# Kernel optimization log

Hardware: AMD Instinct MI355X
Metric: run time of the kernel (lower is better)

Reference implementation:

```python
import jax, jax.numpy as jnp
import numpy as np

DIM = 1024
INTER = 1408
N_EXPERTS = 16
TOPK = 2
N_SHARED = 2
SHARED_INTER = N_SHARED * INTER
ROUTE_SCALE = 1.0


def setup_inputs() -> dict:
    key = jax.random.key(0)
    ks = jax.random.split(key, 16)
    s = 0.02
    return {
        "x": jax.random.normal(ks[0], (2, 2048, DIM), dtype=jnp.float32),
        "gate_w": jax.random.normal(ks[1], (DIM, N_EXPERTS), dtype=jnp.float32) * s,
        "gate_b": jnp.zeros((N_EXPERTS,), dtype=jnp.float32),
        "w1": jax.random.normal(ks[2], (N_EXPERTS, DIM, INTER), dtype=jnp.float32) * s,
        "b1": jnp.zeros((N_EXPERTS, INTER), dtype=jnp.float32),
        "w3": jax.random.normal(ks[3], (N_EXPERTS, DIM, INTER), dtype=jnp.float32) * s,
        "b3": jnp.zeros((N_EXPERTS, INTER), dtype=jnp.float32),
        "w2": jax.random.normal(ks[4], (N_EXPERTS, INTER, DIM), dtype=jnp.float32) * s,
        "b2": jnp.zeros((N_EXPERTS, DIM), dtype=jnp.float32),
        "sw1": jax.random.normal(ks[5], (DIM, SHARED_INTER), dtype=jnp.float32) * s,
        "sb1": jax.random.normal(ks[6], (SHARED_INTER,), dtype=jnp.float32) * s,
        "sw3": jax.random.normal(ks[7], (DIM, SHARED_INTER), dtype=jnp.float32) * s,
        "sb3": jax.random.normal(ks[8], (SHARED_INTER,), dtype=jnp.float32) * s,
        "sw2": jax.random.normal(ks[9], (SHARED_INTER, DIM), dtype=jnp.float32) * s,
        "sb2": jax.random.normal(ks[10], (DIM,), dtype=jnp.float32) * s,
    }


def reference(x, gate_w, gate_b, w1, b1, w3, b3, w2, b2, sw1, sb1, sw3, sb3, sw2, sb2):
    shape = x.shape
    xf = x.reshape(-1, DIM)  # [T, D]

    # Gate: softmax scores in fp32, top-k routing
    logits = xf @ gate_w + gate_b  # [T, E]
    scores = jax.nn.softmax(logits.astype(jnp.float32), axis=-1)
    top_vals, top_idx = jax.lax.top_k(scores, TOPK)  # [T, K]
    weights = (top_vals * ROUTE_SCALE).astype(x.dtype)

    # Combine weights per expert: [T, E]; zero for unselected experts
    cw = (jax.nn.one_hot(top_idx, N_EXPERTS, dtype=x.dtype) * weights[..., None]).sum(axis=1)

    # Routed experts (dense-per-expert SwiGLU, masked by combine weights)
    h = jnp.einsum('td,edh->teh', xf, w1) + b1  # [T, E, I]
    g = jnp.einsum('td,edh->teh', xf, w3) + b3
    a = jax.nn.silu(h) * g
    y = jnp.einsum('teh,ehd,te->td', a, w2, cw) + cw @ b2  # [T, D]

    # Shared expert SwiGLU
    z = (jax.nn.silu(xf @ sw1 + sb1) * (xf @ sw3 + sb3)) @ sw2 + sb2

    return (y + z).reshape(shape)
```

## Files before the change

### kernel.cpp

```cpp
#include <hip/hip_runtime.h>
#include <cstdint>
#include <cstddef>

#define T_TOKENS 4096
#define DIM      1024
#define INTER    1408
#define NEXP     16
#define SINTER   2816

typedef uint32_t u32;
typedef uint16_t u16;

using s8v = __attribute__((ext_vector_type(8))) short;
using f4v = __attribute__((ext_vector_type(4))) float;

__device__ __forceinline__ u16 f2bf(float f) {
  u32 u = __float_as_uint(f);
  return (u16)((u + 0x7fffu + ((u >> 16) & 1u)) >> 16);
}
__device__ __forceinline__ u32 pack2(float a, float b) {
  return (u32)f2bf(a) | ((u32)f2bf(b) << 16);
}

__device__ __forceinline__ void load_lds16(const u16* g, u16* l) {
  __builtin_amdgcn_global_load_lds((const __attribute__((address_space(1))) void*)g,
                                   (__attribute__((address_space(3))) void*)l,
                                   16, 0, 0);
}

__global__ __launch_bounds__(256)
void cvt_x(const float* __restrict__ in, u16* __restrict__ out) {
  const int i = (blockIdx.x * 256 + threadIdx.x) * 8;
  float4 a = *(const float4*)(in + i);
  float4 b = *(const float4*)(in + i + 4);
  uint4 o;
  o.x = pack2(a.x, a.y); o.y = pack2(a.z, a.w);
  o.z = pack2(b.x, b.y); o.w = pack2(b.z, b.w);
  *(uint4*)(out + i) = o;
}

__global__ __launch_bounds__(256)
void transpose_cvt(const float* __restrict__ in, u16* __restrict__ out,
                   int K, int N) {
  const size_t eoff = (size_t)blockIdx.z * K * N;
  const int n0 = blockIdx.x * 64, k0 = blockIdx.y * 64;
  __shared__ u16 t[64][72];

  const int tid = threadIdx.x;
  {
    const int r = tid >> 4, c4 = (tid & 15) * 4;
    const float* src = in + eoff + (size_t)k0 * N + n0;
#pragma unroll
    for (int i = 0; i < 4; i++) {
      int row = r + i * 16;
      float4 v = *(const float4*)(src + (size_t)row * N + c4);
      t[c4 + 0][row] = f2bf(v.x);
      t[c4 + 1][row] = f2bf(v.y);
      t[c4 + 2][row] = f2bf(v.z);
      t[c4 + 3][row] = f2bf(v.w);
    }
  }
  __syncthreads();
  {
    const int r = tid >> 3, cc = (tid & 7) * 8;
    u16* dst = out + eoff + (size_t)n0 * K + k0;
#pragma unroll
    for (int i = 0; i < 2; i++) {
      int row = r + i * 32;
      uint4 v = *(const uint4*)&t[row][cc];
      *(uint4*)(dst + (size_t)row * K + cc) = v;
    }
  }
}

__global__ __launch_bounds__(256)
void gate_logits(const float* __restrict__ x, const float* __restrict__ gw,
                 const float* __restrict__ gb,
                 int* __restrict__ g_e, float* __restrict__ g_w)
{
  const int tok  = blockIdx.x * 4 + (threadIdx.x >> 6);
  const int lane = threadIdx.x & 63;
  const int e = lane & 15, s = lane >> 4;
  const float* xr = x + (size_t)tok * DIM;

  float acc = 0.f;
#pragma unroll 8
  for (int i = 0; i < DIM / 4; i++) {
    const int k = i * 4 + s;
    acc = fmaf(xr[k], gw[i * 64 + lane], acc);
  }
  acc += __shfl_xor(acc, 16, 64);
  acc += __shfl_xor(acc, 32, 64);
  const float logit = acc + gb[e];

  float mx = logit;
#pragma unroll
  for (int o = 1; o < 16; o <<= 1) mx = fmaxf(mx, __shfl_xor(mx, o, 64));
  float p = __expf(logit - mx);
  float sum = p;
#pragma unroll
  for (int o = 1; o < 16; o <<= 1) sum += __shfl_xor(sum, o, 64);
  p /= sum;

  float m0 = p; int i0 = e;
#pragma unroll
  for (int o = 1; o < 16; o <<= 1) {
    float om = __shfl_xor(m0, o, 64); int oi = __shfl_xor(i0, o, 64);
    if (om > m0 || (om == m0 && oi < i0)) { m0 = om; i0 = oi; }
  }
  float p1 = (e == i0) ? -1.f : p;
  float m1 = p1; int i1 = e;
#pragma unroll
  for (int o = 1; o < 16; o <<= 1) {
    float om = __shfl_xor(m1, o, 64); int oi = __shfl_xor(i1, o, 64);
    if (om > m1 || (om == m1 && oi < i1)) { m1 = om; i1 = oi; }
  }
  if (lane == 0) {
    g_e[tok * 2 + 0] = i0;  g_e[tok * 2 + 1] = i1;
    g_w[tok * 2 + 0] = m0;  g_w[tok * 2 + 1] = m1;
  }
}

__global__ __launch_bounds__(256)
void route_build(const int* __restrict__ g_e,
                 int* __restrict__ offsets,
                 int* __restrict__ tok_slot, int* __restrict__ slot_of)
{
  __shared__ int hist[256][NEXP + 1];
  __shared__ int base[NEXP + 1];
  const int tid = threadIdx.x;
  const int TPT = T_TOKENS / 256;
  const int t0 = tid * TPT;

#pragma unroll
  for (int e = 0; e < NEXP; e++) hist[tid][e] = 0;
  for (int t = t0; t < t0 + TPT; t++) {
    hist[tid][g_e[t * 2 + 0]]++;
    hist[tid][g_e[t * 2 + 1]]++;
  }
  __syncthreads();
  if (tid < NEXP) {
    int run = 0;
    for (int i = 0; i < 256; i++) { int v = hist[i][tid]; hist[i][tid] = run; run += v; }
    base[tid] = run;
  }
  __syncthreads();
  if (tid == 0) {
    int run = 0;
#pragma unroll
    for (int e = 0; e < NEXP; e++) { int c = base[e]; base[e] = run; offsets[e] = run; run += c; }
    base[NEXP] = run; offsets[NEXP] = run;
  }
  __syncthreads();
  for (int t = t0; t < t0 + TPT; t++) {
#pragma unroll
    for (int k = 0; k < 2; k++) {
      const int e = g_e[t * 2 + k];
      const int slot = base[e] + hist[tid][e]++;
      tok_slot[slot] = t;
      slot_of[t * 2 + k] = slot;
    }
  }
}

template<bool GATHER>
__global__ __launch_bounds__(256, 2)
void ffn_up4(const u16* __restrict__ xbf,
             const u16* __restrict__ w1t, const float* __restrict__ b1p,
             const u16* __restrict__ w3t, const float* __restrict__ b3p,
             int N,
             const int* __restrict__ offsets, const int* __restrict__ tok_slot,
             u16* __restrict__ act)
{
  const int e = GATHER ? blockIdx.z : 0;
  int rowbase = 0, count = T_TOKENS;
  if constexpr (GATHER) { rowbase = offsets[e]; count = offsets[e + 1] - rowbase; }
  const int m0 = blockIdx.y * 128;
  if (m0 >= count) return;
  const int n0 = blockIdx.x * 128;

  const u16* W1 = w1t + (size_t)e * N * DIM;
  const u16* W3 = w3t + (size_t)e * N * DIM;
  const float* B1 = b1p + (size_t)e * N;
  const float* B3 = b3p + (size_t)e * N;

  __shared__ u16 sA[2][128 * 32];
  __shared__ u16 sB1[2][128 * 32];
  __shared__ u16 sB3[2][128 * 32];

  const int tid = threadIdx.x;
  const int lane = tid & 63;
  const int w = tid >> 6;

  const int kc8 = (lane & 3) * 8;
  const u16* aptr[2]; const u16* b1ptr[2]; const u16* b3ptr[2];
  int ldoff[2];
#pragma unroll
  for (int i = 0; i < 2; i++) {
    const int row = i * 64 + w * 16 + (lane >> 2);
    ldoff[i] = i * 2048 + w * 512 + lane * 8;
    int arow = m0 + row; if (arow > count - 1) arow = count - 1;
    const int tok = GATHER ? tok_slot[rowbase + arow] : arow;
    aptr[i]  = xbf + (size_t)tok * DIM + kc8;
    const int brow = n0 + row;
    b1ptr[i] = W1 + (size_t)brow * DIM + kc8;
    b3ptr[i] = W3 + (size_t)brow * DIM + kc8;
  }

  const int ln = lane & 15, q = lane >> 4;
  const int wm = (w & 1) * 64, wn = (w >> 1) * 64;
  const int paOff = (wm + ln) * 32 + q * 8;
  const int pbOff = (wn + ln) * 32 + q * 8;

  f4v acc1[4][4] = {};
  f4v acc3[4][4] = {};

  auto stage = [&](int buf, int k0) {
#pragma unroll
    for (int i = 0; i < 2; i++) {
      load_lds16(aptr[i]  + k0, &sA[buf][ldoff[i]]);
      load_lds16(b1ptr[i] + k0, &sB1[buf][ldoff[i]]);
      load_lds16(b3ptr[i] + k0, &sB3[buf][ldoff[i]]);
    }
  };

  stage(0, 0);
  __syncthreads();
  int cur = 0;
  for (int k0 = 32; k0 <= DIM; k0 += 32) {
    if (k0 < DIM) stage(cur ^ 1, k0);

    const u16* pa  = sA[cur]  + paOff;
    const u16* pb1 = sB1[cur] + pbOff;
    const u16* pb3 = sB3[cur] + pbOff;
    s8v af[4];
#pragma unroll
    for (int i = 0; i < 4; i++) af[i] = *(const s8v*)(pa + i * 512);
#pragma unroll
    for (int j = 0; j < 4; j++) {
      s8v bf1 = *(const s8v*)(pb1 + j * 512);
#pragma unroll
      for (int i = 0; i < 4; i++)
        acc1[i][j] = __builtin_amdgcn_mfma_f32_16x16x32_bf16(af[i], bf1, acc1[i][j], 0, 0, 0);
      s8v bf3 = *(const s8v*)(pb3 + j * 512);
#pragma unroll
      for (int i = 0; i < 4; i++)
        acc3[i][j] = __builtin_amdgcn_mfma_f32_16x16x32_bf16(af[i], bf3, acc3[i][j], 0, 0, 0);
    }
    __syncthreads();
    cur ^= 1;
  }

  float bb1[4], bb3[4];
#pragma unroll
  for (int j = 0; j < 4; j++) {
    const int col = n0 + wn + j * 16 + ln;
    bb1[j] = B1[col]; bb3[j] = B3[col];
  }
#pragma unroll
  for (int i = 0; i < 4; i++) {
#pragma unroll
    for (int r = 0; r < 4; r++) {
      const int row = m0 + wm + i * 16 + q * 4 + r;
      if (row >= count) continue;
      u16* ap = act + (size_t)(rowbase + row) * N + n0 + wn;
#pragma unroll
      for (int j = 0; j < 4; j++) {
        float h = acc1[i][j][r] + bb1[j];
        float g = acc3[i][j][r] + bb3[j];
        float sv = 1.f / (1.f + __expf(-h));
        ap[j * 16 + ln] = f2bf(h * sv * g);
      }
    }
  }
}

template<bool ROUTED>
__global__ __launch_bounds__(256, 2)
void ffn_down4(const u16* __restrict__ act, int KA,
               const u16* __restrict__ w2t, const float* __restrict__ b2p,
               const int* __restrict__ offsets,
               float* __restrict__ outp)
{
  const int e = ROUTED ? blockIdx.z : 0;
  int rowbase = 0, count = T_TOKENS;
  if constexpr (ROUTED) { rowbase = offsets[e]; count = offsets[e + 1] - rowbase; }
  const int m0 = blockIdx.y * 128;
  if (m0 >= count) return;
  const int n0 = blockIdx.x * 128;

  const u16* W2 = w2t + (size_t)e * DIM * KA;
  const float* B2 = b2p + (size_t)e * DIM;

  __shared__ u16 sA[2][128 * 32];
  __shared__ u16 sB[2][128 * 32];

  const int tid = threadIdx.x;
  const int lane = tid & 63;
  const int w = tid >> 6;

  const int kc8 = (lane & 3) * 8;
  const u16* aptr[2]; const u16* bptr[2];
  int ldoff[2];
#pragma unroll
  for (int i = 0; i < 2; i++) {
    const int row = i * 64 + w * 16 + (lane >> 2);
    ldoff[i] = i * 2048 + w * 512 + lane * 8;
    int arow = m0 + row; if (arow > count - 1) arow = count - 1;
    aptr[i] = act + (size_t)(rowbase + arow) * KA + kc8;
    bptr[i] = W2 + (size_t)(n0 + row) * KA + kc8;
  }

  const int ln = lane & 15, q = lane >> 4;
  const int wm = (w & 1) * 64, wn = (w >> 1) * 64;
  const int paOff = (wm + ln) * 32 + q * 8;
  const int pbOff = (wn + ln) * 32 + q * 8;

  f4v acc[4][4] = {};

  auto stage = [&](int buf, int k0) {
#pragma unroll
    for (int i = 0; i < 2; i++) {
      load_lds16(aptr[i] + k0, &sA[buf][ldoff[i]]);
      load_lds16(bptr[i] + k0, &sB[buf][ldoff[i]]);
    }
  };

  stage(0, 0);
  __syncthreads();
  int cur = 0;
  for (int k0 = 32; k0 <= KA; k0 += 32) {
    if (k0 < KA) stage(cur ^ 1, k0);

    const u16* pa = sA[cur] + paOff;
    const u16* pb = sB[cur] + pbOff;
    s8v af[4];
#pragma unroll
    for (int i = 0; i < 4; i++) af[i] = *(const s8v*)(pa + i * 512);
#pragma unroll
    for (int j = 0; j < 4; j++) {
      s8v bf = *(const s8v*)(pb + j * 512);
#pragma unroll
      for (int i = 0; i < 4; i++)
        acc[i][j] = __builtin_amdgcn_mfma_f32_16x16x32_bf16(af[i], bf, acc[i][j], 0, 0, 0);
    }
    __syncthreads();
    cur ^= 1;
  }

  float bb[4];
#pragma unroll
  for (int j = 0; j < 4; j++) bb[j] = B2[n0 + wn + j * 16 + ln];

#pragma unroll
  for (int i = 0; i < 4; i++) {
#pragma unroll
    for (int r = 0; r < 4; r++) {
      const int row = m0 + wm + i * 16 + q * 4 + r;
      if (row >= count) continue;
      float* orow = outp + (size_t)(rowbase + row) * DIM + n0 + wn;
#pragma unroll
      for (int j = 0; j < 4; j++)
        orow[j * 16 + ln] = acc[i][j][r] + bb[j];
    }
  }
}

__global__ __launch_bounds__(256)
void combine(const float* __restrict__ R, const int* __restrict__ slot_of,
             const float* __restrict__ g_w, float* __restrict__ out)
{
  const int t = blockIdx.x;
  const int c = threadIdx.x * 4;
  const int s0 = slot_of[t * 2 + 0], s1 = slot_of[t * 2 + 1];
  const float w0 = g_w[t * 2 + 0],  w1 = g_w[t * 2 + 1];
  float4 a = *(const float4*)(R + (size_t)s0 * DIM + c);
  float4 b = *(const float4*)(R + (size_t)s1 * DIM + c);
  float* op = out + (size_t)t * DIM + c;
  float4 o = *(const float4*)op;
  o.x += w0 * a.x + w1 * b.x;
  o.y += w0 * a.y + w1 * b.y;
  o.z += w0 * a.z + w1 * b.z;
  o.w += w0 * a.w + w1 * b.w;
  *(float4*)op = o;
}

extern "C" void kernel_launch(void* const* d_in, const int* in_sizes, int n_in,
                              void* d_out, int out_size, void* d_ws, size_t ws_size,
                              hipStream_t stream)
{
  const float* x   = (const float*)d_in[0];
  const float* gw  = (const float*)d_in[1];
  const float* gb  = (const float*)d_in[2];
  const float* w1  = (const float*)d_in[3];
  const float* b1  = (const float*)d_in[4];
  const float* w3  = (const float*)d_in[5];
  const float* b3  = (const float*)d_in[6];
  const float* w2  = (const float*)d_in[7];
  const float* b2  = (const float*)d_in[8];
  const float* sw1 = (const float*)d_in[9];
  const float* sb1 = (const float*)d_in[10];
  const float* sw3 = (const float*)d_in[11];
  const float* sb3 = (const float*)d_in[12];
  const float* sw2 = (const float*)d_in[13];
  const float* sb2 = (const float*)d_in[14];
  float* out = (float*)d_out;

  char* ws = (char*)d_ws;
  size_t off = 0;
  auto alloc = [&](size_t bytes) -> char* {
    off = (off + 255) & ~(size_t)255;
    char* p = ws + off;
    off += bytes;
    return p;
  };
  int*   offsets  = (int*)  alloc((NEXP + 1) * 4);
  int*   g_e      = (int*)  alloc((size_t)T_TOKENS * 2 * 4);
  float* g_w      = (float*)alloc((size_t)T_TOKENS * 2 * 4);
  int*   tok_slot = (int*)  alloc((size_t)T_TOKENS * 2 * 4);
  int*   slot_of  = (int*)  alloc((size_t)T_TOKENS * 2 * 4);
  u16*   xbf      = (u16*)  alloc((size_t)T_TOKENS * DIM * 2);
  u16*   w1t      = (u16*)  alloc((size_t)NEXP * INTER * DIM * 2);
  u16*   w3t      = (u16*)  alloc((size_t)NEXP * INTER * DIM * 2);
  u16*   w2t      = (u16*)  alloc((size_t)NEXP * DIM * INTER * 2);
  u16*   sw1t     = (u16*)  alloc((size_t)SINTER * DIM * 2);
  u16*   sw3t     = (u16*)  alloc((size_t)SINTER * DIM * 2);
  u16*   sw2t     = (u16*)  alloc((size_t)DIM * SINTER * 2);
  u16*   A_act    = (u16*)  alloc((size_t)T_TOKENS * 2 * INTER * 2);
  u16*   S_act    = (u16*)  alloc((size_t)T_TOKENS * SINTER * 2);
  float* Rbuf     = (float*)w1t;
  (void)ws_size; (void)in_sizes; (void)n_in; (void)out_size;

  gate_logits<<<T_TOKENS / 4, 256, 0, stream>>>(x, gw, gb, g_e, g_w);
  route_build<<<1, 256, 0, stream>>>(g_e, offsets, tok_slot, slot_of);

  cvt_x<<<(T_TOKENS * DIM) / (256 * 8), 256, 0, stream>>>(x, xbf);
  transpose_cvt<<<dim3(INTER / 64, DIM / 64, NEXP), 256, 0, stream>>>(w1, w1t, DIM, INTER);
  transpose_cvt<<<dim3(INTER / 64, DIM / 64, NEXP), 256, 0, stream>>>(w3, w3t, DIM, INTER);
  transpose_cvt<<<dim3(DIM / 64, INTER / 64, NEXP), 256, 0, stream>>>(w2, w2t, INTER, DIM);
  transpose_cvt<<<dim3(SINTER / 64, DIM / 64, 1), 256, 0, stream>>>(sw1, sw1t, DIM, SINTER);
  transpose_cvt<<<dim3(SINTER / 64, DIM / 64, 1), 256, 0, stream>>>(sw3, sw3t, DIM, SINTER);
  transpose_cvt<<<dim3(DIM / 64, SINTER / 64, 1), 256, 0, stream>>>(sw2, sw2t, SINTER, DIM);

  ffn_up4<false><<<dim3(SINTER / 128, T_TOKENS / 128, 1), 256, 0, stream>>>(
      xbf, sw1t, sb1, sw3t, sb3, SINTER, nullptr, nullptr, S_act);
  ffn_down4<false><<<dim3(DIM / 128, T_TOKENS / 128, 1), 256, 0, stream>>>(
      S_act, SINTER, sw2t, sb2, nullptr, out);

  ffn_up4<true><<<dim3(INTER / 128, T_TOKENS / 128, NEXP), 256, 0, stream>>>(
      xbf, w1t, b1, w3t, b3, INTER, offsets, tok_slot, A_act);
  ffn_down4<true><<<dim3(DIM / 128, T_TOKENS / 128, NEXP), 256, 0, stream>>>(
      A_act, INTER, w2t, b2, offsets, Rbuf);
  combine<<<T_TOKENS, 256, 0, stream>>>(Rbuf, slot_of, g_w, out);
}
```

Baseline: 694.1 us.

## Merge shared and routed expert GEMMs into single launches with split-K shared down

Merges the shared-expert and routed-expert up-projection GEMMs into one launch, with an extra z-slice for the shared expert, and does the same for the down-projection. The shared down-projection is split along K into two halves written to separate partial buffers, which the combine kernel then sums. The w1/w3 weight transposes are also paired into single launches. The aim is to cut launch count and fill the GPU better by running shared and routed work concurrently. In exchange it writes and reads extra fp32 partial buffers, and the routed up launch now includes many blocks that exit early.

```diff
diff --git a/kernel.cpp b/kernel.cpp
--- a/kernel.cpp
+++ b/kernel.cpp
@@ -7,6 +7,7 @@
 #define INTER    1408
 #define NEXP     16
 #define SINTER   2816
+#define KD       1408
 
 typedef uint32_t u32;
 typedef uint16_t u16;
@@ -37,6 +38,44 @@
   o.x = pack2(a.x, a.y); o.y = pack2(a.z, a.w);
   o.z = pack2(b.x, b.y); o.w = pack2(b.z, b.w);
   *(uint4*)(out + i) = o;
+}
+
+__global__ __launch_bounds__(256)
+void transpose_cvt2(const float* __restrict__ in0, const float* __restrict__ in1,
+                    u16* __restrict__ out0, u16* __restrict__ out1,
+                    int K, int N) {
+  const int e = blockIdx.z >> 1, sel = blockIdx.z & 1;
+  const float* in = sel ? in1 : in0;
+  u16* out = sel ? out1 : out0;
+  const size_t eoff = (size_t)e * K * N;
+  const int n0 = blockIdx.x * 64, k0 = blockIdx.y * 64;
+  __shared__ u16 t[64][72];
+
+  const int tid = threadIdx.x;
+  {
+    const int r = tid >> 4, c4 = (tid & 15) * 4;
+    const float* src = in + eoff + (size_t)k0 * N + n0;
+#pragma unroll
+    for (int i = 0; i < 4; i++) {
+      int row = r + i * 16;
+      float4 v = *(const float4*)(src + (size_t)row * N + c4);
+      t[c4 + 0][row] = f2bf(v.x);
+      t[c4 + 1][row] = f2bf(v.y);
+      t[c4 + 2][row] = f2bf(v.z);
+      t[c4 + 3][row] = f2bf(v.w);
+    }
+  }
+  __syncthreads();
+  {
+    const int r = tid >> 3, cc = (tid & 7) * 8;
+    u16* dst = out + eoff + (size_t)n0 * K + k0;
+#pragma unroll
+    for (int i = 0; i < 2; i++) {
+      int row = r + i * 32;
+      uint4 v = *(const uint4*)&t[row][cc];
+      *(uint4*)(dst + (size_t)row * K + cc) = v;
+    }
+  }
 }
 
 __global__ __launch_bounds__(256)
@@ -163,26 +202,32 @@
   }
 }
 
-template<bool GATHER>
 __global__ __launch_bounds__(256, 2)
-void ffn_up4(const u16* __restrict__ xbf,
-             const u16* __restrict__ w1t, const float* __restrict__ b1p,
-             const u16* __restrict__ w3t, const float* __restrict__ b3p,
-             int N,
-             const int* __restrict__ offsets, const int* __restrict__ tok_slot,
-             u16* __restrict__ act)
+void ffn_up_m(const u16* __restrict__ xbf,
+              const u16* __restrict__ w1t, const float* __restrict__ b1p,
+              const u16* __restrict__ w3t, const float* __restrict__ b3p,
+              const u16* __restrict__ sw1t, const float* __restrict__ sb1,
+              const u16* __restrict__ sw3t, const float* __restrict__ sb3,
+              const int* __restrict__ offsets, const int* __restrict__ tok_slot,
+              u16* __restrict__ A_act, u16* __restrict__ S_act)
 {
-  const int e = GATHER ? blockIdx.z : 0;
-  int rowbase = 0, count = T_TOKENS;
-  if constexpr (GATHER) { rowbase = offsets[e]; count = offsets[e + 1] - rowbase; }
+  const int z = blockIdx.z;
+  const bool shr = (z == NEXP);
+  int N, count, rowbase = 0;
+  const u16 *W1, *W3; const float *B1, *B3; u16* act;
+  if (shr) {
+    N = SINTER; count = T_TOKENS;
+    W1 = sw1t; W3 = sw3t; B1 = sb1; B3 = sb3; act = S_act;
+  } else {
+    N = INTER; rowbase = offsets[z]; count = offsets[z + 1] - rowbase;
+    W1 = w1t + (size_t)z * INTER * DIM; W3 = w3t + (size_t)z * INTER * DIM;
+    B1 = b1p + (size_t)z * INTER;       B3 = b3p + (size_t)z * INTER;
+    act = A_act;
+  }
+  const int n0 = blockIdx.x * 128;
+  if (n0 >= N) return;
   const int m0 = blockIdx.y * 128;
   if (m0 >= count) return;
-  const int n0 = blockIdx.x * 128;
-
-  const u16* W1 = w1t + (size_t)e * N * DIM;
-  const u16* W3 = w3t + (size_t)e * N * DIM;
-  const float* B1 = b1p + (size_t)e * N;
-  const float* B3 = b3p + (size_t)e * N;
 
   __shared__ u16 sA[2][128 * 32];
   __shared__ u16 sB1[2][128 * 32];
@@ -200,7 +245,7 @@
     const int row = i * 64 + w * 16 + (lane >> 2);
     ldoff[i] = i * 2048 + w * 512 + lane * 8;
     int arow = m0 + row; if (arow > count - 1) arow = count - 1;
-    const int tok = GATHER ? tok_slot[rowbase + arow] : arow;
+    const int tok = shr ? arow : tok_slot[rowbase + arow];
     aptr[i]  = xbf + (size_t)tok * DIM + kc8;
     const int brow = n0 + row;
     b1ptr[i] = W1 + (size_t)brow * DIM + kc8;
@@ -275,22 +320,33 @@
   }
 }
 
-template<bool ROUTED>
 __global__ __launch_bounds__(256, 2)
-void ffn_down4(const u16* __restrict__ act, int KA,
-               const u16* __restrict__ w2t, const float* __restrict__ b2p,
-               const int* __restrict__ offsets,
-               float* __restrict__ outp)
+void ffn_down_m(const u16* __restrict__ A_act, const u16* __restrict__ S_act,
+                const u16* __restrict__ w2t, const float* __restrict__ b2p,
+                const u16* __restrict__ sw2t, const float* __restrict__ sb2,
+                const int* __restrict__ offsets,
+                float* __restrict__ Rbuf, float* __restrict__ Spart)
 {
-  const int e = ROUTED ? blockIdx.z : 0;
-  int rowbase = 0, count = T_TOKENS;
-  if constexpr (ROUTED) { rowbase = offsets[e]; count = offsets[e + 1] - rowbase; }
+  const int z = blockIdx.z;
+  int count, rowbase = 0, astride, koff;
+  const u16 *Abase, *W2; const float* B2; float* outp; bool addBias; int ostride_base;
+  if (z < NEXP) {
+    rowbase = offsets[z]; count = offsets[z + 1] - rowbase;
+    Abase = A_act; astride = INTER; koff = 0;
+    W2 = w2t + (size_t)z * DIM * INTER;
+    B2 = b2p + (size_t)z * DIM; addBias = true;
+    outp = Rbuf; ostride_base = rowbase;
+  } else {
+    const int h = z - NEXP;
+    count = T_TOKENS;
+    Abase = S_act; astride = SINTER; koff = h * KD;
+    W2 = sw2t;
+    B2 = sb2; addBias = (h == 0);
+    outp = Spart + (size_t)h * T_TOKENS * DIM; ostride_base = 0;
+  }
   const int m0 = blockIdx.y * 128;
   if (m0 >= count) return;
   const int n0 = blockIdx.x * 128;
-
-  const u16* W2 = w2t + (size_t)e * DIM * KA;
-  const float* B2 = b2p + (size_t)e * DIM;
 
   __shared__ u16 sA[2][128 * 32];
   __shared__ u16 sB[2][128 * 32];
@@ -307,8 +363,8 @@
     const int row = i * 64 + w * 16 + (lane >> 2);
     ldoff[i] = i * 2048 + w * 512 + lane * 8;
     int arow = m0 + row; if (arow > count - 1) arow = count - 1;
-    aptr[i] = act + (size_t)(rowbase + arow) * KA + kc8;
-    bptr[i] = W2 + (size_t)(n0 + row) * KA + kc8;
+    aptr[i] = Abase + (size_t)(rowbase + arow) * astride + koff + kc8;
+    bptr[i] = W2 + (size_t)(n0 + row) * astride + koff + kc8;
   }
 
   const int ln = lane & 15, q = lane >> 4;
@@ -329,8 +385,8 @@
   stage(0, 0);
   __syncthreads();
   int cur = 0;
-  for (int k0 = 32; k0 <= KA; k0 += 32) {
-    if (k0 < KA) stage(cur ^ 1, k0);
+  for (int k0 = 32; k0 <= KD; k0 += 32) {
+    if (k0 < KD) stage(cur ^ 1, k0);
 
     const u16* pa = sA[cur] + paOff;
     const u16* pb = sB[cur] + pbOff;
@@ -350,7 +406,7 @@
 
   float bb[4];
 #pragma unroll
-  for (int j = 0; j < 4; j++) bb[j] = B2[n0 + wn + j * 16 + ln];
+  for (int j = 0; j < 4; j++) bb[j] = addBias ? B2[n0 + wn + j * 16 + ln] : 0.f;
 
 #pragma unroll
   for (int i = 0; i < 4; i++) {
@@ -358,7 +414,7 @@
     for (int r = 0; r < 4; r++) {
       const int row = m0 + wm + i * 16 + q * 4 + r;
       if (row >= count) continue;
-      float* orow = outp + (size_t)(rowbase + row) * DIM + n0 + wn;
+      float* orow = outp + (size_t)(ostride_base + row) * DIM + n0 + wn;
 #pragma unroll
       for (int j = 0; j < 4; j++)
         orow[j * 16 + ln] = acc[i][j][r] + bb[j];
@@ -367,7 +423,8 @@
 }
 
 __global__ __launch_bounds__(256)
-void combine(const float* __restrict__ R, const int* __restrict__ slot_of,
+void combine(const float* __restrict__ R, const float* __restrict__ Spart,
+             const int* __restrict__ slot_of,
              const float* __restrict__ g_w, float* __restrict__ out)
 {
   const int t = blockIdx.x;
@@ -376,13 +433,14 @@
   const float w0 = g_w[t * 2 + 0],  w1 = g_w[t * 2 + 1];
   float4 a = *(const float4*)(R + (size_t)s0 * DIM + c);
   float4 b = *(const float4*)(R + (size_t)s1 * DIM + c);
-  float* op = out + (size_t)t * DIM + c;
-  float4 o = *(const float4*)op;
-  o.x += w0 * a.x + w1 * b.x;
-  o.y += w0 * a.y + w1 * b.y;
-  o.z += w0 * a.z + w1 * b.z;
-  o.w += w0 * a.w + w1 * b.w;
-  *(float4*)op = o;
+  float4 p = *(const float4*)(Spart + (size_t)t * DIM + c);
+  float4 qq = *(const float4*)(Spart + (size_t)(T_TOKENS + t) * DIM + c);
+  float4 o;
+  o.x = p.x + qq.x + w0 * a.x + w1 * b.x;
+  o.y = p.y + qq.y + w0 * a.y + w1 * b.y;
+  o.z = p.z + qq.z + w0 * a.z + w1 * b.z;
+  o.w = p.w + qq.w + w0 * a.w + w1 * b.w;
+  *(float4*)(out + (size_t)t * DIM + c) = o;
 }
 
 extern "C" void kernel_launch(void* const* d_in, const int* in_sizes, int n_in,
@@ -429,27 +487,26 @@
   u16*   A_act    = (u16*)  alloc((size_t)T_TOKENS * 2 * INTER * 2);
   u16*   S_act    = (u16*)  alloc((size_t)T_TOKENS * SINTER * 2);
   float* Rbuf     = (float*)w1t;
+  float* Spart    = (float*)w3t;
   (void)ws_size; (void)in_sizes; (void)n_in; (void)out_size;
 
   gate_logits<<<T_TOKENS / 4, 256, 0, stream>>>(x, gw, gb, g_e, g_w);
   route_build<<<1, 256, 0, stream>>>(g_e, offsets, tok_slot, slot_of);
 
   cvt_x<<<(T_TOKENS * DIM) / (256 * 8), 256, 0, stream>>>(x, xbf);
-  transpose_cvt<<<dim3(INTER / 64, DIM / 64, NEXP), 256, 0, stream>>>(w1, w1t, DIM, INTER);
-  transpose_cvt<<<dim3(INTER / 64, DIM / 64, NEXP), 256, 0, stream>>>(w3, w3t, DIM, INTER);
+  transpose_cvt2<<<dim3(INTER / 64, DIM / 64, 2 * NEXP), 256, 0, stream>>>(
+      w1, w3, w1t, w3t, DIM, INTER);
   transpose_cvt<<<dim3(DIM / 64, INTER / 64, NEXP), 256, 0, stream>>>(w2, w2t, INTER, DIM);
-  transpose_cvt<<<dim3(SINTER / 64, DIM / 64, 1), 256, 0, stream>>>(sw1, sw1t, DIM, SINTER);
-  transpose_cvt<<<dim3(SINTER / 64, DIM / 64, 1), 256, 0, stream>>>(sw3, sw3t, DIM, SINTER);
+  transpose_cvt2<<<dim3(SINTER / 64, DIM / 64, 2), 256, 0, stream>>>(
+      sw1, sw3, sw1t, sw3t, DIM, SINTER);
   transpose_cvt<<<dim3(DIM / 64, SINTER / 64, 1), 256, 0, stream>>>(sw2, sw2t, SINTER, DIM);
 
-  ffn_up4<false><<<dim3(SINTER / 128, T_TOKENS / 128, 1), 256, 0, stream>>>(
-      xbf, sw1t, sb1, sw3t, sb3, SINTER, nullptr, nullptr, S_act);
-  ffn_down4<false><<<dim3(DIM / 128, T_TOKENS / 128, 1), 256, 0, stream>>>(
-      S_act, SINTER, sw2t, sb2, nullptr, out);
-
-  ffn_up4<true><<<dim3(INTER / 128, T_TOKENS / 128, NEXP), 256, 0, stream>>>(
-      xbf, w1t, b1, w3t, b3, INTER, offsets, tok_slot, A_act);
-  ffn_down4<true><<<dim3(DIM / 128, T_TOKENS / 128, NEXP), 256, 0, stream>>>(
-      A_act, INTER, w2t, b2, offsets, Rbuf);
-  combine<<<T_TOKENS, 256, 0, stream>>>(Rbuf, slot_of, g_w, out);
-}
+  ffn_up_m<<<dim3(SINTER / 128, T_TOKENS / 128, NEXP + 1), 256, 0, stream>>>(
+      xbf, w1t, b1, w3t, b3, sw1t, sb1, sw3t, sb3,
+      offsets, tok_slot, A_act, S_act);
+
+  ffn_down_m<<<dim3(DIM / 128, T_TOKENS / 128, NEXP + 2), 256, 0, stream>>>(
+      A_act, S_act, w2t, b2, sw2t, sb2, offsets, Rbuf, Spart);
+
+  combine<<<T_TOKENS, 256, 0, stream>>>(Rbuf, Spart, slot_of, g_w, out);
+}
```

Measured after the change: 653.7 us. 1.06x faster.
